# Performance work log

Measured on AMD Instinct MI355X. Metric: run time of the kernel, lower is better.

Reference implementation:

```python
import jax, jax.numpy as jnp
import numpy as np

K = 20  # number of nearest neighbors (includes self, distance 0, as in torch topk(largest=False))


def edge_feature(x, k):
    """x: (B, C, N) -> edge features (B, N, k, 2C) = concat[central, neighbor - central]."""
    sq = jnp.sum(x * x, axis=1)                       # (B, N)
    inner = jnp.einsum('bcn,bcm->bnm', x, x)          # (B, N, N)
    d = sq[:, :, None] + sq[:, None, :] - 2.0 * inner # squared pairwise distance
    _, idx = jax.lax.top_k(-d, k)                     # (B, N, k) nearest indices (incl. self)
    xT = jnp.transpose(x, (0, 2, 1))                  # (B, N, C)
    # nb[b,n,j,c] = xT[b, idx[b,n,j], c]
    nb = jnp.take_along_axis(xT[:, :, None, :], idx[:, :, :, None], axis=1)  # (B, N, k, C)
    central = jnp.broadcast_to(xT[:, :, None, :], nb.shape)
    return jnp.concatenate([central, nb - central], axis=-1)  # (B, N, k, 2C)


def setup_inputs() -> dict:
    key = jax.random.key(0)
    ks = jax.random.split(key, 13)
    B, C, N = 8, 3, 4096
    def w(k_, shape, fan_in):
        return (jax.random.normal(k_, shape, dtype=jnp.float32) / np.sqrt(fan_in)).astype(jnp.float32)
    inp = {
        'x':  jax.random.normal(ks[0], (B, C, N), dtype=jnp.float32),
        # local 1x1 conv2d weights (out_ch, in_ch)
        'W1': w(ks[1], (64, 6), 6),        'b1': jnp.zeros((64,), jnp.float32),
        'W2': w(ks[2], (128, 64), 64),     'b2': jnp.zeros((128,), jnp.float32),
        # inter 1x1 conv1d
        'W3': w(ks[3], (1024, 128), 128),  'b3': jnp.zeros((1024,), jnp.float32),
        # global FC
        'W4': w(ks[4], (512, 1024), 1024), 'b4': jnp.zeros((512,), jnp.float32),
        'W5': w(ks[5], (256, 512), 512),   'b5': jnp.zeros((256,), jnp.float32),
        # final linear (torch inits this to zeros -> identity output; use small random for a
        # non-trivial correctness baseline, same math path)
        'W6': 0.01 * w(ks[6], (9, 256), 256), 'b6': jnp.zeros((9,), jnp.float32),
    }
    return inp


def reference(x, W1, b1, W2, b2, W3, b3, W4, b4, W5, b5, W6, b6):
    e = edge_feature(x, K)                                     # (B, N, k, 6)
    h = jax.nn.relu(jnp.einsum('bnkc,oc->bnko', e, W1) + b1)   # (B, N, k, 64)
    h = jax.nn.relu(jnp.einsum('bnkc,oc->bnko', h, W2) + b2)   # (B, N, k, 128)
    h = jnp.max(h, axis=2)                                     # max over k -> (B, N, 128)
    h = jax.nn.relu(jnp.einsum('bnc,oc->bno', h, W3) + b3)     # (B, N, 1024)
    g = jnp.max(h, axis=1)                                     # max over points -> (B, 1024)
    g = jax.nn.relu(g @ W4.T + b4)                             # (B, 512)
    g = jax.nn.relu(g @ W5.T + b5)                             # (B, 256)
    t = g @ W6.T + b6                                          # (B, 9)
    Bsz = x.shape[0]
    out_ch, in_ch = 3, 3
    t = t.reshape(Bsz, out_ch, in_ch) + jnp.eye(out_ch, in_ch, dtype=t.dtype)
    return t
```

## Files before the change

kernel.cpp:

```cpp
#include <hip/hip_runtime.h>
#include <hip/hip_bf16.h>
#include <cstdint>

#define B_SZ 8
#define NPTS 4096
#define KNN  20
#define NTOT (B_SZ * NPTS)
#define PPB  8

typedef unsigned int uint;
typedef unsigned short ushort;
using short8 = __attribute__((ext_vector_type(8))) short;
using f32x4  = __attribute__((ext_vector_type(4))) float;

__device__ __forceinline__ ushort f2bf(float f) {
  uint u = __float_as_uint(f);
  u += 0x7fff + ((u >> 16) & 1);
  return (ushort)(u >> 16);
}
__device__ __forceinline__ float bf2f(ushort h) {
  return __uint_as_float(((uint)h) << 16);
}

__global__ __launch_bounds__(256) void prep_kernel(const float* __restrict__ x,
                                                   const float* __restrict__ W1,
                                                   const float* __restrict__ W3,
                                                   ushort* __restrict__ u,
                                                   ushort* __restrict__ W3b) {
  int blk = blockIdx.x;
  if (blk < 8192) {
    int t = blk * 256 + threadIdx.x;
    int p = t >> 6, o = t & 63;
    int b = p >> 12, n = p & (NPTS - 1);
    const float* xb = x + (size_t)b * 3 * NPTS;
    float x0 = xb[n], x1 = xb[NPTS + n], x2 = xb[2 * NPTS + n];
    const float* w = W1 + o * 6;
    u[t] = f2bf(w[3] * x0 + w[4] * x1 + w[5] * x2);
  } else {
    int t = (blk - 8192) * 256 + threadIdx.x;
    const float4* src = reinterpret_cast<const float4*>(W3 + t * 8);
    float4 f0 = src[0], f1 = src[1];
    uint4 pk;
    pk.x = (uint)f2bf(f0.x) | ((uint)f2bf(f0.y) << 16);
    pk.y = (uint)f2bf(f0.z) | ((uint)f2bf(f0.w) << 16);
    pk.z = (uint)f2bf(f1.x) | ((uint)f2bf(f1.y) << 16);
    pk.w = (uint)f2bf(f1.z) | ((uint)f2bf(f1.w) << 16);
    *reinterpret_cast<uint4*>(W3b + t * 8) = pk;
  }
}

__device__ __forceinline__ void sortf64(float& v, int lane) {
  #pragma unroll
  for (int k = 2; k <= 64; k <<= 1) {
    #pragma unroll
    for (int j = k >> 1; j > 0; j >>= 1) {
      float o = __shfl_xor(v, j, 64);
      bool keepmin = (((lane & k) == 0) == ((lane & j) == 0));
      bool lt = v < o;
      v = (keepmin == lt) ? v : o;
    }
  }
}

__device__ __forceinline__ void sortu64(unsigned long long& v, int lane) {
  #pragma unroll
  for (int k = 2; k <= 64; k <<= 1) {
    #pragma unroll
    for (int j = k >> 1; j > 0; j >>= 1) {
      unsigned long long o = __shfl_xor(v, j, 64);
      bool keepmin = (((lane & k) == 0) == ((lane & j) == 0));
      bool lt = v < o;
      v = (keepmin == lt) ? v : o;
    }
  }
}

__global__ __launch_bounds__(256, 4) void knn_kernel(const float* __restrict__ x,
                                                     int* __restrict__ idx_out) {
  __shared__ int surv[4][256];
  __shared__ int cnt[4];
  const unsigned long long INFK = ~0ull;
  int w = threadIdx.x >> 6, lane = threadIdx.x & 63;
  int row = blockIdx.x * 4 + w;
  int b = row >> 12, n = row & (NPTS - 1);
  const float* xb = x + (size_t)b * 3 * NPTS;
  float qx = xb[n], qy = xb[NPTS + n], qz = xb[2 * NPTS + n];
  if (lane == 0) cnt[w] = 0;

  const float4* X0 = reinterpret_cast<const float4*>(xb);
  const float4* X1 = reinterpret_cast<const float4*>(xb + NPTS);
  const float4* X2 = reinterpret_cast<const float4*>(xb + 2 * NPTS);

  uint kreg[32];
  float bm = 3.0e38f;
  #pragma unroll
  for (int i = 0; i < 16; ++i) {
    int v4 = i * 64 + lane;
    float4 a0 = X0[v4], a1 = X1[v4], a2 = X2[v4];
    float dx, dy, dz, d0, d1, d2, d3;
    dx = a0.x - qx; dy = a1.x - qy; dz = a2.x - qz; d0 = dx*dx + dy*dy + dz*dz;
    dx = a0.y - qx; dy = a1.y - qy; dz = a2.y - qz; d1 = dx*dx + dy*dy + dz*dz;
    dx = a0.z - qx; dy = a1.z - qy; dz = a2.z - qz; d2 = dx*dx + dy*dy + dz*dz;
    dx = a0.w - qx; dy = a1.w - qy; dz = a2.w - qz; d3 = dx*dx + dy*dy + dz*dz;
    bm = fminf(bm, fminf(fminf(d0, d1), fminf(d2, d3)));
    kreg[2*i]   = (__float_as_uint(d0) >> 16) | (__float_as_uint(d1) & 0xFFFF0000u);
    kreg[2*i+1] = (__float_as_uint(d2) >> 16) | (__float_as_uint(d3) & 0xFFFF0000u);
  }

  sortf64(bm, lane);
  float T = __shfl(bm, 19, 64);
  uint T16 = __float_as_uint(T) >> 16;

  asm volatile("s_waitcnt lgkmcnt(0)" ::: "memory");
  #pragma unroll
  for (int i = 0; i < 16; ++i) {
    uint ka = kreg[2*i], kb = kreg[2*i+1];
    uint h0 = ((ka & 0xffffu) <= T16) ? 1u : 0u;
    uint h1 = ((ka >> 16)     <= T16) ? 1u : 0u;
    uint h2 = ((kb & 0xffffu) <= T16) ? 1u : 0u;
    uint h3 = ((kb >> 16)     <= T16) ? 1u : 0u;
    uint h = h0 + h1 + h2 + h3;
    if (h) {
      int s = atomicAdd(&cnt[w], (int)h);
      int m0 = (i * 64 + lane) * 4;
      if (h0) { if (s < 256) surv[w][s] = m0;     s++; }
      if (h1) { if (s < 256) surv[w][s] = m0 + 1; s++; }
      if (h2) { if (s < 256) surv[w][s] = m0 + 2; s++; }
      if (h3) { if (s < 256) surv[w][s] = m0 + 3; s++; }
    }
  }
  asm volatile("s_waitcnt lgkmcnt(0)" ::: "memory");
  int M = cnt[w];

  if (M <= 256) {
    unsigned long long run = INFK;
    int nch = (M + 63) >> 6;
    for (int c = 0; c < nch; ++c) {
      int s = c * 64 + lane;
      unsigned long long v = INFK;
      if (s < M) {
        int m = surv[w][s];
        float dx = xb[m] - qx, dy = xb[NPTS + m] - qy, dz = xb[2 * NPTS + m] - qz;
        float d = dx * dx + dy * dy + dz * dz;
        v = ((unsigned long long)__float_as_uint(d) << 32) | (unsigned)m;
      }
      sortu64(v, lane);
      if (c == 0) {
        run = v;
      } else {
        unsigned long long b19 = __shfl(v, (19 - lane) & 63, 64);
        unsigned long long cand = run < b19 ? run : b19;
        run = (lane < KNN) ? cand : INFK;
        sortu64(run, lane);
      }
    }
    if (lane < KNN) idx_out[(size_t)row * KNN + lane] = (int)(run & 0xFFFFFFFFull);
  } else {
    unsigned long long prev = 0ull;
    for (int r = 0; r < KNN; ++r) {
      unsigned long long best = INFK;
      for (int i = 0; i < 16; ++i) {
        int v4 = i * 64 + lane;
        float4 a0 = X0[v4], a1 = X1[v4], a2 = X2[v4];
        float dx, dy, dz, d[4];
        dx = a0.x - qx; dy = a1.x - qy; dz = a2.x - qz; d[0] = dx*dx + dy*dy + dz*dz;
        dx = a0.y - qx; dy = a1.y - qy; dz = a2.y - qz; d[1] = dx*dx + dy*dy + dz*dz;
        dx = a0.z - qx; dy = a1.z - qy; dz = a2.z - qz; d[2] = dx*dx + dy*dy + dz*dz;
        dx = a0.w - qx; dy = a1.w - qy; dz = a2.w - qz; d[3] = dx*dx + dy*dy + dz*dz;
        #pragma unroll
        for (int j = 0; j < 4; ++j) {
          int m = i * 256 + lane * 4 + j;
          unsigned long long key =
              ((unsigned long long)__float_as_uint(d[j]) << 32) | (unsigned)m;
          if ((r == 0 || key > prev) && key < best) best = key;
        }
      }
      #pragma unroll
      for (int off = 32; off; off >>= 1) {
        unsigned long long o = __shfl_xor(best, off, 64);
        best = o < best ? o : best;
      }
      if (lane == 0) idx_out[(size_t)row * KNN + r] = (int)(best & 0xFFFFFFFFull);
      prev = best;
    }
  }
}

__global__ __launch_bounds__(256, 2) void edge_kernel(
    const float* __restrict__ x,  const float* __restrict__ W1, const float* __restrict__ b1,
    const float* __restrict__ W2, const float* __restrict__ b2,
    const ushort* __restrict__ u, const int* __restrict__ idx,
    float* __restrict__ h128) {
  __shared__ __align__(16) char w2s[128 * 128];
  __shared__ __align__(16) char h1s[PPB * 32 * 128];
  __shared__ float vs[PPB * 64];
  __shared__ int   nbs[PPB * KNN];

  int tid = threadIdx.x, w = tid >> 6, l = tid & 63;
  int p0 = blockIdx.x * PPB;
  int b = p0 >> 12;
  const float* xb = x + (size_t)b * 3 * NPTS;

  for (int e = tid; e < 1024; e += 256) {
    int row = e >> 3, c0 = (e & 7) * 8;
    const float* wp = W2 + row * 64 + c0;
    float4 f0 = *(const float4*)wp, f1 = *(const float4*)(wp + 4);
    uint4 pk;
    pk.x = (uint)f2bf(f0.x) | ((uint)f2bf(f0.y) << 16);
    pk.y = (uint)f2bf(f0.z) | ((uint)f2bf(f0.w) << 16);
    pk.z = (uint)f2bf(f1.x) | ((uint)f2bf(f1.y) << 16);
    pk.w = (uint)f2bf(f1.z) | ((uint)f2bf(f1.w) << 16);
    int byte = (row * 128 + c0 * 2) ^ ((row & 7) << 4);
    *(uint4*)(w2s + byte) = pk;
  }
  for (int t = tid; t < PPB * 64; t += 256) {
    int p = t >> 6, c = t & 63;
    int n = (p0 + p) & (NPTS - 1);
    float x0 = xb[n], x1 = xb[NPTS + n], x2 = xb[2 * NPTS + n];
    const float* wr = W1 + c * 6;
    vs[t] = (wr[0] - wr[3]) * x0 + (wr[1] - wr[4]) * x1 + (wr[2] - wr[5]) * x2 + b1[c];
  }
  if (tid < PPB * KNN) nbs[tid] = idx[(size_t)p0 * KNN + tid];
  __syncthreads();

  const ushort* ub = u + (((size_t)b) << 12) * 64;
  #pragma unroll
  for (int j = 0; j < 8; ++j) {
    int e_loc = j * 8 + (l >> 3);
    int p_loc = (w << 1) + (e_loc >> 5);
    int e_in = e_loc & 31;
    int e_src = (e_in < KNN) ? e_in : e_in - KNN;
    int nb = nbs[p_loc * KNN + e_src];
    int c0 = (l & 7) * 8;
    uint4 uv = *(const uint4*)(ub + (((size_t)nb) << 6) + c0);
    const float* vp = vs + p_loc * 64 + c0;
    float4 v0 = *(const float4*)vp, v1 = *(const float4*)(vp + 4);
    float h0 = fmaxf(bf2f((ushort)(uv.x & 0xffff)) + v0.x, 0.f);
    float h1 = fmaxf(bf2f((ushort)(uv.x >> 16))    + v0.y, 0.f);
    float h2 = fmaxf(bf2f((ushort)(uv.y & 0xffff)) + v0.z, 0.f);
    float h3 = fmaxf(bf2f((ushort)(uv.y >> 16))    + v0.w, 0.f);
    float h4 = fmaxf(bf2f((ushort)(uv.z & 0xffff)) + v1.x, 0.f);
    float h5 = fmaxf(bf2f((ushort)(uv.z >> 16))    + v1.y, 0.f);
    float h6 = fmaxf(bf2f((ushort)(uv.w & 0xffff)) + v1.z, 0.f);
    float h7 = fmaxf(bf2f((ushort)(uv.w >> 16))    + v1.w, 0.f);
    uint4 pk;
    pk.x = (uint)f2bf(h0) | ((uint)f2bf(h1) << 16);
    pk.y = (uint)f2bf(h2) | ((uint)f2bf(h3) << 16);
    pk.z = (uint)f2bf(h4) | ((uint)f2bf(h5) << 16);
    pk.w = (uint)f2bf(h6) | ((uint)f2bf(h7) << 16);
    int row = (w << 6) + e_loc;
    int byte = (row * 128 + c0 * 2) ^ ((row & 7) << 4);
    *(uint4*)(h1s + byte) = pk;
  }
  __syncthreads();

  short8 bfr[8][2];
  #pragma unroll
  for (int nt = 0; nt < 8; ++nt) {
    #pragma unroll
    for (int ks = 0; ks < 2; ++ks) {
      int row = nt * 16 + (l & 15);
      int byte = (row * 128 + ks * 64 + (l >> 4) * 16) ^ ((row & 7) << 4);
      bfr[nt][ks] = *(const short8*)(w2s + byte);
    }
  }
  float bias0 = b2[l], bias1 = b2[64 + l];

  #pragma unroll
  for (int pt = 0; pt < 2; ++pt) {
    int rbase = (w << 6) + (pt << 5);
    short8 a[2][2];
    #pragma unroll
    for (int m = 0; m < 2; ++m) {
      #pragma unroll
      for (int ks = 0; ks < 2; ++ks) {
        int row = rbase + m * 16 + (l & 15);
        int byte = (row * 128 + ks * 64 + (l >> 4) * 16) ^ ((row & 7) << 4);
        a[m][ks] = *(const short8*)(h1s + byte);
      }
    }
    float r03 = 0.f, r47 = 0.f;
    #pragma unroll
    for (int nt = 0; nt < 8; ++nt) {
      f32x4 acc0 = {0.f, 0.f, 0.f, 0.f}, acc1 = {0.f, 0.f, 0.f, 0.f};
      acc0 = __builtin_amdgcn_mfma_f32_16x16x32_bf16(a[0][0], bfr[nt][0], acc0, 0, 0, 0);
      acc0 = __builtin_amdgcn_mfma_f32_16x16x32_bf16(a[0][1], bfr[nt][1], acc0, 0, 0, 0);
      acc1 = __builtin_amdgcn_mfma_f32_16x16x32_bf16(a[1][0], bfr[nt][0], acc1, 0, 0, 0);
      acc1 = __builtin_amdgcn_mfma_f32_16x16x32_bf16(a[1][1], bfr[nt][1], acc1, 0, 0, 0);
      float m0 = fmaxf(fmaxf(fmaxf(acc0[0], acc1[0]), fmaxf(acc0[1], acc1[1])),
                       fmaxf(fmaxf(acc0[2], acc1[2]), fmaxf(acc0[3], acc1[3])));
      m0 = fmaxf(m0, __shfl_xor(m0, 16, 64));
      m0 = fmaxf(m0, __shfl_xor(m0, 32, 64));
      if ((l >> 4) == (nt & 3)) { if (nt < 4) r03 = m0; else r47 = m0; }
    }
    int pg = p0 + (w << 1) + pt;
    h128[(size_t)pg * 128 + l]      = fmaxf(r03 + bias0, 0.f);
    h128[(size_t)pg * 128 + 64 + l] = fmaxf(r47 + bias1, 0.f);
  }
}

__global__ __launch_bounds__(256, 2) void inter_kernel(
    const float* __restrict__ h128, const ushort* __restrict__ W3b,
    float* __restrict__ partial) {
  __shared__ __align__(16) char as_[32 * 256];
  int tid = threadIdx.x, w = tid >> 6, l = tid & 63;
  int chunk = blockIdx.x;
  const float* hp = h128 + (size_t)chunk * 32 * 128;

  {
    int row = tid >> 3, c0 = (tid & 7) * 16;
    const float4* src = reinterpret_cast<const float4*>(hp + row * 128 + c0);
    float4 f0 = src[0], f1 = src[1], f2 = src[2], f3 = src[3];
    uint4 p0, p1;
    p0.x = (uint)f2bf(f0.x) | ((uint)f2bf(f0.y) << 16);
    p0.y = (uint)f2bf(f0.z) | ((uint)f2bf(f0.w) << 16);
    p0.z = (uint)f2bf(f1.x) | ((uint)f2bf(f1.y) << 16);
    p0.w = (uint)f2bf(f1.z) | ((uint)f2bf(f1.w) << 16);
    p1.x = (uint)f2bf(f2.x) | ((uint)f2bf(f2.y) << 16);
    p1.y = (uint)f2bf(f2.z) | ((uint)f2bf(f2.w) << 16);
    p1.z = (uint)f2bf(f3.x) | ((uint)f2bf(f3.y) << 16);
    p1.w = (uint)f2bf(f3.z) | ((uint)f2bf(f3.w) << 16);
    int sw = (row & 7) << 4;
    *(uint4*)(as_ + ((row * 256 + c0 * 2) ^ sw))      = p0;
    *(uint4*)(as_ + ((row * 256 + c0 * 2 + 16) ^ sw)) = p1;
  }
  __syncthreads();

  short8 a[2][4];
  #pragma unroll
  for (int m = 0; m < 2; ++m) {
    #pragma unroll
    for (int ks = 0; ks < 4; ++ks) {
      int row = m * 16 + (l & 15);
      int byte = (row * 256 + ks * 64 + (l >> 4) * 16) ^ ((row & 7) << 4);
      a[m][ks] = *(const short8*)(as_ + byte);
    }
  }

  const ushort* wb = W3b + (size_t)(w * 256) * 128;
  float res[4];
  #pragma unroll
  for (int nt = 0; nt < 16; ++nt) {
    f32x4 acc0 = {0.f, 0.f, 0.f, 0.f}, acc1 = {0.f, 0.f, 0.f, 0.f};
    #pragma unroll
    for (int ks = 0; ks < 4; ++ks) {
      short8 bf = *(const short8*)(wb + (size_t)(nt * 16 + (l & 15)) * 128
                                      + ks * 32 + (l >> 4) * 8);
      acc0 = __builtin_amdgcn_mfma_f32_16x16x32_bf16(a[0][ks], bf, acc0, 0, 0, 0);
      acc1 = __builtin_amdgcn_mfma_f32_16x16x32_bf16(a[1][ks], bf, acc1, 0, 0, 0);
    }
    float m0 = fmaxf(fmaxf(fmaxf(acc0[0], acc1[0]), fmaxf(acc0[1], acc1[1])),
                     fmaxf(fmaxf(acc0[2], acc1[2]), fmaxf(acc0[3], acc1[3])));
    m0 = fmaxf(m0, __shfl_xor(m0, 16, 64));
    m0 = fmaxf(m0, __shfl_xor(m0, 32, 64));
    if ((l >> 4) == (nt & 3)) res[nt >> 2] = m0;
  }
  float* pp = partial + (size_t)chunk * 1024 + w * 256;
  #pragma unroll
  for (int g = 0; g < 4; ++g) pp[g * 64 + l] = res[g];
}

__global__ __launch_bounds__(256) void gmax_kernel(const float* __restrict__ partial,
                                                   const float* __restrict__ b3,
                                                   float* __restrict__ g) {
  int t = blockIdx.x * 256 + threadIdx.x;
  if (t >= B_SZ * 1024) return;
  int b = t >> 10, ch = t & 1023;
  const float* p = partial + (size_t)b * 128 * 1024 + ch;
  float m = -3.0e38f;
  for (int i = 0; i < 128; ++i) m = fmaxf(m, p[(size_t)i * 1024]);
  g[t] = fmaxf(m + b3[ch], 0.0f);
}

__global__ __launch_bounds__(64) void fc_kernel(const float* __restrict__ in,
                                                const float* __restrict__ W,
                                                const float* __restrict__ bias,
                                                float* __restrict__ out,
                                                int in_dim, int out_dim, int mode) {
  int blk = blockIdx.x;
  int b = blk / out_dim, o = blk % out_dim;
  int lane = threadIdx.x;
  const float* iv = in + (size_t)b * in_dim;
  const float* w  = W  + (size_t)o * in_dim;
  float s = 0.f;
  for (int c = lane; c < in_dim; c += 64) s += iv[c] * w[c];
  #pragma unroll
  for (int off = 32; off; off >>= 1) s += __shfl_down(s, off);
  if (lane == 0) {
    float r = s + bias[o];
    if (mode == 0) r = fmaxf(r, 0.0f);
    else if (o == 0 || o == 4 || o == 8) r += 1.0f;
    out[blk] = r;
  }
}

extern "C" void kernel_launch(void* const* d_in, const int* in_sizes, int n_in,
                              void* d_out, int out_size, void* d_ws, size_t ws_size,
                              hipStream_t stream) {
  const float* x  = (const float*)d_in[0];
  const float* W1 = (const float*)d_in[1];
  const float* b1 = (const float*)d_in[2];
  const float* W2 = (const float*)d_in[3];
  const float* b2 = (const float*)d_in[4];
  const float* W3 = (const float*)d_in[5];
  const float* b3 = (const float*)d_in[6];
  const float* W4 = (const float*)d_in[7];
  const float* b4 = (const float*)d_in[8];
  const float* W5 = (const float*)d_in[9];
  const float* b5 = (const float*)d_in[10];
  const float* W6 = (const float*)d_in[11];
  const float* b6 = (const float*)d_in[12];
  float* out = (float*)d_out;

  char* ws = (char*)d_ws;
  ushort* u_bf = (ushort*)(ws);
  int*   idxb  = (int*)  (ws + (8u  << 20));
  float* h128  = (float*)(ws + (11u << 20));
  ushort* W3b  = (ushort*)(ws + (27u << 20));
  float* part  = (float*)(ws);
  float* g     = (float*)(ws + (5u  << 20));
  float* g4    = (float*)(ws + (6u  << 20));
  float* g5    = (float*)(ws + (7u  << 20));

  hipLaunchKernelGGL(prep_kernel, dim3(8256), dim3(256), 0, stream, x, W1, W3, u_bf, W3b);
  hipLaunchKernelGGL(knn_kernel,  dim3(8192), dim3(256), 0, stream, x, idxb);
  hipLaunchKernelGGL(edge_kernel, dim3(NTOT / PPB), dim3(256), 0, stream,
                     x, W1, b1, W2, b2, u_bf, idxb, h128);
  hipLaunchKernelGGL(inter_kernel, dim3(1024), dim3(256), 0, stream, h128, W3b, part);
  hipLaunchKernelGGL(gmax_kernel, dim3(32), dim3(256), 0, stream, part, b3, g);
  hipLaunchKernelGGL(fc_kernel, dim3(B_SZ * 512), dim3(64), 0, stream, g,  W4, b4, g4, 1024, 512, 0);
  hipLaunchKernelGGL(fc_kernel, dim3(B_SZ * 256), dim3(64), 0, stream, g4, W5, b5, g5, 512, 256, 0);
  hipLaunchKernelGGL(fc_kernel, dim3(B_SZ * 9),   dim3(64), 0, stream, g5, W6, b6, out, 256, 9, 1);
}
```

Before: 185.3 us.

## Split each KNN query row across two waves and vectorize prep stores

The KNN kernel now gives each query point a 128-thread block of two waves. Each wave scans half the candidate points, and they combine their 20th-smallest thresholds and survivor lists through shared memory with block barriers. This halves the per-wave distance scan and register footprint to cut per-row latency, but the final survivor sort runs redundantly in both waves. The prep kernel also computes 8 bf16 outputs per thread and writes them as one 16-byte store, using far fewer blocks.

New measurement: 194.6 us. +5.1%, slower.

```diff
diff --git a/kernel.cpp b/kernel.cpp
--- a/kernel.cpp
+++ b/kernel.cpp
@@ -28,16 +28,24 @@
                                                    ushort* __restrict__ u,
                                                    ushort* __restrict__ W3b) {
   int blk = blockIdx.x;
-  if (blk < 8192) {
+  if (blk < 1024) {
     int t = blk * 256 + threadIdx.x;
-    int p = t >> 6, o = t & 63;
+    int p = t >> 3, c0 = (t & 7) * 8;
     int b = p >> 12, n = p & (NPTS - 1);
     const float* xb = x + (size_t)b * 3 * NPTS;
     float x0 = xb[n], x1 = xb[NPTS + n], x2 = xb[2 * NPTS + n];
-    const float* w = W1 + o * 6;
-    u[t] = f2bf(w[3] * x0 + w[4] * x1 + w[5] * x2);
+    uint pk[4];
+    #pragma unroll
+    for (int j = 0; j < 8; ++j) {
+      const float* w = W1 + (c0 + j) * 6;
+      float v = w[3] * x0 + w[4] * x1 + w[5] * x2;
+      ushort h = f2bf(v);
+      if (j & 1) pk[j >> 1] |= ((uint)h << 16); else pk[j >> 1] = h;
+    }
+    uint4 q; q.x = pk[0]; q.y = pk[1]; q.z = pk[2]; q.w = pk[3];
+    *reinterpret_cast<uint4*>(u + (size_t)p * 64 + c0) = q;
   } else {
-    int t = (blk - 8192) * 256 + threadIdx.x;
+    int t = (blk - 1024) * 256 + threadIdx.x;
     const float4* src = reinterpret_cast<const float4*>(W3 + t * 8);
     float4 f0 = src[0], f1 = src[1];
     uint4 pk;
@@ -75,27 +83,29 @@
   }
 }
 
-__global__ __launch_bounds__(256, 4) void knn_kernel(const float* __restrict__ x,
+__global__ __launch_bounds__(128, 4) void knn_kernel(const float* __restrict__ x,
                                                      int* __restrict__ idx_out) {
-  __shared__ int surv[4][256];
-  __shared__ int cnt[4];
+  __shared__ int surv[256];
+  __shared__ int cnt;
+  __shared__ float tsh[2];
+  __shared__ unsigned long long fbx[2];
   const unsigned long long INFK = ~0ull;
-  int w = threadIdx.x >> 6, lane = threadIdx.x & 63;
-  int row = blockIdx.x * 4 + w;
+  int half = threadIdx.x >> 6, lane = threadIdx.x & 63;
+  int row = blockIdx.x;
   int b = row >> 12, n = row & (NPTS - 1);
   const float* xb = x + (size_t)b * 3 * NPTS;
   float qx = xb[n], qy = xb[NPTS + n], qz = xb[2 * NPTS + n];
-  if (lane == 0) cnt[w] = 0;
+  if (threadIdx.x == 0) cnt = 0;
 
   const float4* X0 = reinterpret_cast<const float4*>(xb);
   const float4* X1 = reinterpret_cast<const float4*>(xb + NPTS);
   const float4* X2 = reinterpret_cast<const float4*>(xb + 2 * NPTS);
 
-  uint kreg[32];
+  uint kreg[16];
   float bm = 3.0e38f;
   #pragma unroll
-  for (int i = 0; i < 16; ++i) {
-    int v4 = i * 64 + lane;
+  for (int i = 0; i < 8; ++i) {
+    int v4 = half * 512 + i * 64 + lane;
     float4 a0 = X0[v4], a1 = X1[v4], a2 = X2[v4];
     float dx, dy, dz, d0, d1, d2, d3;
     dx = a0.x - qx; dy = a1.x - qy; dz = a2.x - qz; d0 = dx*dx + dy*dy + dz*dz;
@@ -108,12 +118,13 @@
   }
 
   sortf64(bm, lane);
-  float T = __shfl(bm, 19, 64);
+  if (lane == 19) tsh[half] = bm;
+  __syncthreads();
+  float T = fminf(tsh[0], tsh[1]);
   uint T16 = __float_as_uint(T) >> 16;
 
-  asm volatile("s_waitcnt lgkmcnt(0)" ::: "memory");
-  #pragma unroll
-  for (int i = 0; i < 16; ++i) {
+  #pragma unroll
+  for (int i = 0; i < 8; ++i) {
     uint ka = kreg[2*i], kb = kreg[2*i+1];
     uint h0 = ((ka & 0xffffu) <= T16) ? 1u : 0u;
     uint h1 = ((ka >> 16)     <= T16) ? 1u : 0u;
@@ -121,16 +132,16 @@
     uint h3 = ((kb >> 16)     <= T16) ? 1u : 0u;
     uint h = h0 + h1 + h2 + h3;
     if (h) {
-      int s = atomicAdd(&cnt[w], (int)h);
-      int m0 = (i * 64 + lane) * 4;
-      if (h0) { if (s < 256) surv[w][s] = m0;     s++; }
-      if (h1) { if (s < 256) surv[w][s] = m0 + 1; s++; }
-      if (h2) { if (s < 256) surv[w][s] = m0 + 2; s++; }
-      if (h3) { if (s < 256) surv[w][s] = m0 + 3; s++; }
-    }
-  }
-  asm volatile("s_waitcnt lgkmcnt(0)" ::: "memory");
-  int M = cnt[w];
+      int s = atomicAdd(&cnt, (int)h);
+      int m0 = (half * 512 + i * 64 + lane) * 4;
+      if (h0) { if (s < 256) surv[s] = m0;     s++; }
+      if (h1) { if (s < 256) surv[s] = m0 + 1; s++; }
+      if (h2) { if (s < 256) surv[s] = m0 + 2; s++; }
+      if (h3) { if (s < 256) surv[s] = m0 + 3; s++; }
+    }
+  }
+  __syncthreads();
+  int M = cnt;
 
   if (M <= 256) {
     unsigned long long run = INFK;
@@ -139,7 +150,7 @@
       int s = c * 64 + lane;
       unsigned long long v = INFK;
       if (s < M) {
-        int m = surv[w][s];
+        int m = surv[s];
         float dx = xb[m] - qx, dy = xb[NPTS + m] - qy, dz = xb[2 * NPTS + m] - qz;
         float d = dx * dx + dy * dy + dz * dz;
         v = ((unsigned long long)__float_as_uint(d) << 32) | (unsigned)m;
@@ -154,13 +165,14 @@
         sortu64(run, lane);
       }
     }
-    if (lane < KNN) idx_out[(size_t)row * KNN + lane] = (int)(run & 0xFFFFFFFFull);
+    if (half == 0 && lane < KNN)
+      idx_out[(size_t)row * KNN + lane] = (int)(run & 0xFFFFFFFFull);
   } else {
     unsigned long long prev = 0ull;
     for (int r = 0; r < KNN; ++r) {
       unsigned long long best = INFK;
-      for (int i = 0; i < 16; ++i) {
-        int v4 = i * 64 + lane;
+      for (int i = 0; i < 8; ++i) {
+        int v4 = half * 512 + i * 64 + lane;
         float4 a0 = X0[v4], a1 = X1[v4], a2 = X2[v4];
         float dx, dy, dz, d[4];
         dx = a0.x - qx; dy = a1.x - qy; dz = a2.x - qz; d[0] = dx*dx + dy*dy + dz*dz;
@@ -169,7 +181,7 @@
         dx = a0.w - qx; dy = a1.w - qy; dz = a2.w - qz; d[3] = dx*dx + dy*dy + dz*dz;
         #pragma unroll
         for (int j = 0; j < 4; ++j) {
-          int m = i * 256 + lane * 4 + j;
+          int m = v4 * 4 + j;
           unsigned long long key =
               ((unsigned long long)__float_as_uint(d[j]) << 32) | (unsigned)m;
           if ((r == 0 || key > prev) && key < best) best = key;
@@ -180,8 +192,12 @@
         unsigned long long o = __shfl_xor(best, off, 64);
         best = o < best ? o : best;
       }
-      if (lane == 0) idx_out[(size_t)row * KNN + r] = (int)(best & 0xFFFFFFFFull);
-      prev = best;
+      if (lane == 0) fbx[half] = best;
+      __syncthreads();
+      unsigned long long g = fbx[0] < fbx[1] ? fbx[0] : fbx[1];
+      if (threadIdx.x == 0) idx_out[(size_t)row * KNN + r] = (int)(g & 0xFFFFFFFFull);
+      prev = g;
+      __syncthreads();
     }
   }
 }
@@ -422,8 +438,8 @@
   float* g4    = (float*)(ws + (6u  << 20));
   float* g5    = (float*)(ws + (7u  << 20));
 
-  hipLaunchKernelGGL(prep_kernel, dim3(8256), dim3(256), 0, stream, x, W1, W3, u_bf, W3b);
-  hipLaunchKernelGGL(knn_kernel,  dim3(8192), dim3(256), 0, stream, x, idxb);
+  hipLaunchKernelGGL(prep_kernel, dim3(1088), dim3(256), 0, stream, x, W1, W3, u_bf, W3b);
+  hipLaunchKernelGGL(knn_kernel,  dim3(32768), dim3(128), 0, stream, x, idxb);
   hipLaunchKernelGGL(edge_kernel, dim3(NTOT / PPB), dim3(256), 0, stream,
                      x, W1, b1, W2, b2, u_bf, idxb, h128);
   hipLaunchKernelGGL(inter_kernel, dim3(1024), dim3(256), 0, stream, h128, W3b, part);
```
